# Optimization experiments

Measured on AMD Instinct MI355X. Metric: run time of the kernel, lower is better.

## Reference

```python
import jax, jax.numpy as jnp
import numpy as np

B, N, NC = 8, 25200, 80           # YOLOv5-640 / COCO raw output
CONF_THRES = 0.25                  # init conf_threshold
IOU_THRES = 0.45                   # init iou_threshold
PATCH_CONF = 0.001                 # hard-coded patch_conf in forward
GN = jnp.array([640.0, 640.0, 640.0, 640.0], dtype=jnp.float32)  # img_size[[1,0,1,0]]
MAX_WH = 4096.0                    # class offset for class-aware NMS
K_CLEAN = 512                      # fixed-size cap on NMS candidates (clean branch)
K_PATCH = 1024                     # fixed-size cap on NMS candidates (patch branch)
MAX_DET_CLEAN = 1000
MAX_DET_PATCH = 30000
NEG = jnp.float32(-1e30)


def _xywh2xyxy(x):
    xy, wh = x[..., :2], x[..., 2:4]
    return jnp.concatenate([xy - wh * 0.5, xy + wh * 0.5], axis=-1)


def _pairwise_iou(a, b):
    # a: [A,4] xyxy, b: [B,4] xyxy -> [A,B] jaccard overlap
    tl = jnp.maximum(a[:, None, :2], b[None, :, :2])
    br = jnp.minimum(a[:, None, 2:4], b[None, :, 2:4])
    wh = jnp.clip(br - tl, 0.0)
    inter = wh[..., 0] * wh[..., 1]
    area_a = (a[:, 2] - a[:, 0]) * (a[:, 3] - a[:, 1])
    area_b = (b[:, 2] - b[:, 0]) * (b[:, 3] - b[:, 1])
    union = area_a[:, None] + area_b[None, :] - inter
    union = jnp.where(union > 0, union, 1.0)  # guard degenerate boxes
    return inter / union


def _nms_single(pred, conf_thres, K, max_det):
    # pred: [N, 5+nc]. Fixed-size (padded/masked) greedy NMS, class-aware via MAX_WH offset.
    obj = pred[:, 4]
    cls_conf = pred[:, 5:] * obj[:, None]          # x[:,5:] *= x[:,4:5]
    conf = jnp.max(cls_conf, axis=-1)
    cls = jnp.argmax(cls_conf, axis=-1)
    box = _xywh2xyxy(pred[:, :4])
    valid = (obj > conf_thres) & (conf > conf_thres)
    scores = jnp.where(valid, conf, NEG)
    top_scores, idx = jax.lax.top_k(scores, K)     # sorted desc, like torchvision NMS ordering
    boxes = box[idx]
    cls_k = cls[idx]
    valid_k = top_scores > conf_thres
    boxes_off = boxes + cls_k.astype(boxes.dtype)[:, None] * MAX_WH
    iou = jax.lax.stop_gradient(_pairwise_iou(boxes_off, boxes_off))
    ar = jnp.arange(K)

    def step(keep, i):
        sup = keep[i] & (iou[i] > IOU_THRES) & (ar > i)
        return keep & (~sup), None

    keep, _ = jax.lax.scan(step, valid_k, jnp.arange(K))
    rank = jnp.cumsum(keep.astype(jnp.int32))
    keep = keep & (rank <= max_det)
    return boxes, cls_k, keep


def _image_loss(cb, cc, ck, pb, pc, pk):
    # per clean detection: max IoU over kept patch boxes of the same class (0 if none)
    iou = _pairwise_iou(cb / GN, pb / GN)          # [K_CLEAN, K_PATCH]
    mask = ck[:, None] & pk[None, :] & (cc[:, None] == pc[None, :])
    tm = jnp.max(jnp.where(mask, iou, 0.0), axis=1)
    s = jnp.sum(jnp.where(ck, tm, 0.0))
    n = jnp.sum(ck.astype(jnp.float32))
    return s, n


def _forward(output_clean, output_patch):
    cb, cc, ck = jax.vmap(lambda p: _nms_single(p, CONF_THRES, K_CLEAN, MAX_DET_CLEAN))(output_clean)
    pb, pc, pk = jax.vmap(lambda p: _nms_single(p, PATCH_CONF, K_PATCH, MAX_DET_PATCH))(output_patch)
    s, n = jax.vmap(_image_loss)(cb, cc, ck, pb, pc, pk)
    total, cnt = jnp.sum(s), jnp.sum(n)
    return jnp.where(cnt > 0, 1.0 - total / jnp.maximum(cnt, 1.0), jnp.float32(1.0))


def _make_pred(key):
    ka, kb, kc, kd = jax.random.split(key, 4)
    cxcy = jax.random.uniform(ka, (B, N, 2), jnp.float32, 20.0, 620.0)
    wh = jax.random.uniform(kb, (B, N, 2), jnp.float32, 2.0, 150.0)
    obj = jax.random.uniform(kc, (B, N, 1), jnp.float32)
    clsp = jax.random.uniform(kd, (B, N, NC), jnp.float32)
    return jnp.concatenate([cxcy, wh, obj, clsp], axis=-1)


def setup_inputs() -> dict:
    key = jax.random.key(0)
    k1, k2 = jax.random.split(key)
    return {"output_clean": _make_pred(k1), "output_patch": _make_pred(k2)}


def reference(output_clean, output_patch):
    return _forward(output_clean, output_patch)
```

## Files before the change

kernel.cpp:

```cpp
#include <hip/hip_runtime.h>


static constexpr int NB   = 8;
static constexpr int NA   = 25200;
static constexpr int NCLS = 80;
static constexpr int CH   = 85;
static constexpr int NT   = 16;
static constexpr int KMAX = 1024;
static constexpr int NBIN = 32768;
static constexpr int PSH  = 17;
static constexpr int CAP  = 2048;
static constexpr int CPAD = 32;
static constexpr int IOB  = 34;

static constexpr size_t OFF_KEYS = 0;
static constexpr size_t OFF_CLS  = OFF_KEYS + (size_t)NT * NA * 4;
static constexpr size_t OFF_BOX  = OFF_CLS  + (size_t)NT * NA * 4;
static constexpr size_t OFF_CLSK = OFF_BOX  + (size_t)NT * KMAX * 16;
static constexpr size_t OFF_VALK = OFF_CLSK + (size_t)NT * KMAX * 4;
static constexpr size_t OFF_KEEP = OFF_VALK + (size_t)NT * KMAX * 4;
static constexpr size_t OFF_SUP  = OFF_KEEP + (size_t)NT * 16 * 8;
static constexpr size_t OFF_DIAG = OFF_SUP  + (size_t)NT * KMAX * 16 * 8;
static constexpr size_t OFF_PART = OFF_DIAG + (size_t)NT * KMAX * 8;
static constexpr size_t OFF_CNT  = OFF_PART + 512;
static constexpr size_t OFF_THR  = OFF_CNT  + (size_t)NT * 2 * CPAD * 4;
static constexpr size_t OFF_CAND = OFF_THR  + 128;

__device__ __forceinline__ unsigned okey(float f) {
  unsigned u = __float_as_uint(f);
  return (u & 0x80000000u) ? ~u : (u | 0x80000000u);
}

__global__ __launch_bounds__(256) void k_score(const float* __restrict__ clean,
                                               const float* __restrict__ patch,
                                               unsigned* __restrict__ keys,
                                               int* __restrict__ clsArr) {
#pragma clang fp contract(off)
  const int t  = blockIdx.y;
  const int a0 = blockIdx.x * 64;
  const int nA = (NA - a0 < 64) ? (NA - a0) : 64;
  const float conf_th = (t < 8) ? 0.25f : 0.001f;
  const float* __restrict__ src = ((t < 8) ? clean : patch) + (size_t)(t & 7) * NA * CH;
  __shared__ float rows[64 * CH];
  const float4* g4 = (const float4*)(src + (size_t)a0 * CH);
  float4* s4 = (float4*)rows;
  const int n4 = (nA * CH) >> 2;
  for (int i = threadIdx.x; i < n4; i += 256) s4[i] = g4[i];
  __syncthreads();

  const int ar = threadIdx.x >> 2;
  const int q  = threadIdx.x & 3;
  if (ar < nA) {
    const float* r = rows + ar * CH;
    const float obj = r[4];
    const int c0 = q * 20;
    float best = r[5 + c0] * obj;
    int bc = c0;
    for (int c = c0 + 1; c < c0 + 20; ++c) {
      float v = r[5 + c] * obj;
      if (v > best) { best = v; bc = c; }
    }
    {
      float b2 = __shfl_down(best, 2); int c2 = __shfl_down(bc, 2);
      if (b2 > best || (b2 == best && c2 < bc)) { best = b2; bc = c2; }
      float b1 = __shfl_down(best, 1); int c1 = __shfl_down(bc, 1);
      if (b1 > best || (b1 == best && c1 < bc)) { best = b1; bc = c1; }
    }
    if (q == 0) {
      const bool valid = (obj > conf_th) && (best > conf_th);
      const float score = valid ? best : -1e30f;
      const int a = a0 + ar;
      keys[(size_t)t * NA + a]   = okey(score);
      clsArr[(size_t)t * NA + a] = bc;
    }
  }
}

__global__ __launch_bounds__(1024) void k_histsel(const unsigned* __restrict__ keys,
                                                  unsigned* __restrict__ thr,
                                                  unsigned* __restrict__ cnt) {
  const int t = blockIdx.x;
  const unsigned K = (t < 8) ? 512u : 1024u;
  __shared__ unsigned h32[NBIN / 2];
  __shared__ unsigned csum[1024];
  __shared__ int s_chunk;
  __shared__ unsigned s_acc;
  const int tid = threadIdx.x;
  for (int i = tid; i < NBIN / 2; i += 1024) h32[i] = 0u;
  if (tid < 2) cnt[(t * 2 + tid) * CPAD] = 0u;
  __syncthreads();
  const unsigned INVKEY = okey(-1e30f);
  const unsigned* kv = keys + (size_t)t * NA;
  const int lane = tid & 63;
  for (int i = tid; i < NA; i += 1024) {
    unsigned key = kv[i];
    bool inv = (key == INVKEY);
    unsigned long long mb = __ballot(inv);
    if (!inv) {
      unsigned b = key >> PSH;
      atomicAdd(&h32[b >> 1], 1u << ((b & 1) * 16));
    } else if (lane == (int)__ffsll(mb) - 1) {
      unsigned b = INVKEY >> PSH;
      atomicAdd(&h32[b >> 1], (unsigned)__popcll(mb) << ((b & 1) * 16));
    }
  }
  __syncthreads();
  {
    unsigned sum = 0;
    for (int i = 0; i < 16; ++i) {
      unsigned v = h32[tid * 16 + i];
      sum += (v & 0xFFFFu) + (v >> 16);
    }
    csum[tid] = sum;
  }
  __syncthreads();
  for (int off = 1; off < 1024; off <<= 1) {
    unsigned v = csum[tid];
    if (tid + off < 1024) v += csum[tid + off];
    __syncthreads();
    csum[tid] = v;
    __syncthreads();
  }
  {
    bool pred = csum[tid] >= K;
    bool next = (tid == 1023) ? false : (csum[tid + 1] >= K);
    if (pred && !next) {
      s_chunk = tid;
      s_acc = (tid == 1023) ? 0u : csum[tid + 1];
    }
  }
  __syncthreads();
  if (tid == 0) {
    unsigned acc = s_acc;
    unsigned res = (unsigned)(s_chunk * 32);
    for (int i = 31; i >= 0; --i) {
      int bb = s_chunk * 32 + i;
      unsigned v = h32[bb >> 1];
      unsigned c2 = (bb & 1) ? (v >> 16) : (v & 0xFFFFu);
      if (acc + c2 >= K) { res = (unsigned)bb; break; }
      acc += c2;
    }
    thr[t] = res;
  }
}

__global__ __launch_bounds__(256) void k_compact(const unsigned* __restrict__ keys,
                                                 const unsigned* __restrict__ thr,
                                                 unsigned* __restrict__ cnt,
                                                 unsigned long long* __restrict__ cand) {
  const int t = blockIdx.y;
  const int a = blockIdx.x * 256 + threadIdx.x;
  const unsigned B = thr[t];
  unsigned key = 0u, p = 0u;
  const bool inb = (a < NA);
  if (inb) { key = keys[(size_t)t * NA + a]; p = key >> PSH; }
  const bool hi = inb && (p > B);
  const bool eq = inb && (p == B);
  const unsigned long long item =
      ((unsigned long long)key << 32) | (unsigned)(~(unsigned)a);
  const int lane = threadIdx.x & 63;
  const unsigned long long lowmask =
      (lane == 0) ? 0ull : (0xFFFFFFFFFFFFFFFFull >> (64 - lane));
  unsigned long long mh = __ballot(hi);
  if (mh) {
    const int leader = (int)__ffsll(mh) - 1;
    unsigned base = 0;
    if (lane == leader) base = atomicAdd(&cnt[(t * 2 + 0) * CPAD], (unsigned)__popcll(mh));
    base = __shfl(base, leader);
    if (hi) {
      unsigned pos = base + (unsigned)__popcll(mh & lowmask);
      if (pos < 1024u) cand[(size_t)t * CAP + pos] = item;
    }
  }
  unsigned long long me = __ballot(eq);
  if (me) {
    const int leader = (int)__ffsll(me) - 1;
    unsigned base = 0;
    if (lane == leader) base = atomicAdd(&cnt[(t * 2 + 1) * CPAD], (unsigned)__popcll(me));
    base = __shfl(base, leader);
    if (eq) {
      unsigned pos = base + (unsigned)__popcll(me & lowmask);
      if (pos < 1024u) cand[(size_t)t * CAP + 1024 + pos] = item;
    }
  }
}

__global__ __launch_bounds__(1024) void k_sort(const float* __restrict__ clean,
                                               const float* __restrict__ patch,
                                               const unsigned* __restrict__ cnt,
                                               const unsigned long long* __restrict__ cand,
                                               const int* __restrict__ clsArr,
                                               float* __restrict__ boxesK,
                                               int* __restrict__ clsK,
                                               int* __restrict__ validK) {
#pragma clang fp contract(off)
  const int t = blockIdx.x;
  const int K = (t < 8) ? 512 : 1024;
  const float conf_th = (t < 8) ? 0.25f : 0.001f;
  __shared__ unsigned long long buf[CAP];
  const unsigned nHi = min(cnt[(t * 2 + 0) * CPAD], 1024u);
  const unsigned nEq = min(cnt[(t * 2 + 1) * CPAD], 1024u);
  const unsigned long long* cd = cand + (size_t)t * CAP;
  for (int i = threadIdx.x; i < CAP; i += 1024) {
    unsigned long long v = 0ull;
    if (i < 1024) { if ((unsigned)i < nHi) v = cd[i]; }
    else          { if ((unsigned)(i - 1024) < nEq) v = cd[i]; }
    buf[i] = v;
  }
  __syncthreads();
  for (int kk2 = 2; kk2 <= CAP; kk2 <<= 1) {
    for (int j = kk2 >> 1; j > 0; j >>= 1) {
      for (int i = threadIdx.x; i < CAP; i += 1024) {
        int ixj = i ^ j;
        if (ixj > i) {
          unsigned long long a = buf[i], b = buf[ixj];
          bool desc = ((i & kk2) == 0);
          if (desc ? (a < b) : (a > b)) { buf[i] = b; buf[ixj] = a; }
        }
      }
      __syncthreads();
    }
  }
  const float* __restrict__ src = ((t < 8) ? clean : patch) + (size_t)(t & 7) * NA * CH;
  const unsigned vkey = okey(conf_th);
  for (int k = threadIdx.x; k < K; k += 1024) {
    unsigned long long v = buf[k];
    unsigned key = (unsigned)(v >> 32);
    int idx = (int)(~(unsigned)(v & 0xFFFFFFFFull));
    if (idx < 0) idx = 0;
    const float* r = src + (size_t)idx * CH;
    float cx = r[0], cy = r[1], w = r[2], h = r[3];
    float hw = w * 0.5f, hh = h * 0.5f;
    float* bo = boxesK + ((size_t)t * KMAX + k) * 4;
    bo[0] = cx - hw; bo[1] = cy - hh; bo[2] = cx + hw; bo[3] = cy + hh;
    clsK[t * KMAX + k]   = clsArr[(size_t)t * NA + idx];
    validK[t * KMAX + k] = (key > vkey) ? 1 : 0;
  }
}

__global__ __launch_bounds__(256) void k_ioumat(const float* __restrict__ boxesK,
                                                const int* __restrict__ clsK,
                                                unsigned long long* __restrict__ sup,
                                                unsigned long long* __restrict__ diag) {
#pragma clang fp contract(off)
  const int t  = blockIdx.y;
  const int K  = (t < 8) ? 512 : 1024;
  const int lw = (t < 8) ? 3 : 4;
  const int nw = 1 << lw;
  const int npair = (nw * (nw + 1)) / 2;
  const int total = npair * 64;
  if (blockIdx.x * 256 >= total) return;
  __shared__ float X1[KMAX + 16], Y1[KMAX + 16], X2[KMAX + 16], Y2[KMAX + 16], AR[KMAX + 16];
  for (int i = threadIdx.x; i < K; i += 256) {
    const float* bo = boxesK + ((size_t)t * KMAX + i) * 4;
    float off = (float)clsK[t * KMAX + i] * 4096.0f;
    float x1 = bo[0] + off, y1 = bo[1] + off, x2 = bo[2] + off, y2 = bo[3] + off;
    const int ip = i + (i >> 6);
    X1[ip] = x1; Y1[ip] = y1; X2[ip] = x2; Y2[ip] = y2;
    AR[ip] = (x2 - x1) * (y2 - y1);
  }
  __syncthreads();
  unsigned long long* supt = sup + (size_t)t * (KMAX * 16);
  for (int widx = blockIdx.x * 256 + threadIdx.x; widx < total; widx += IOB * 256) {
    int p = widx >> 6;
    int row = widx & 63;
    int rb = 0, pr = p;
    while (pr >= nw - rb) { pr -= nw - rb; ++rb; }
    const int wc = rb + pr;
    const int i = rb * 64 + row;
    const int ipi = i + rb;
    const float x1i = X1[ipi], y1i = Y1[ipi], x2i = X2[ipi], y2i = Y2[ipi], ai = AR[ipi];
    unsigned long long m = 0ull;
    const int jb = (wc << 6) + wc;
    const bool offd = (wc > rb);
#pragma unroll 4
    for (int l = 0; l < 64; ++l) {
      const int jp = jb + l;
      float tlx = fmaxf(x1i, X1[jp]);
      float tly = fmaxf(y1i, Y1[jp]);
      float brx = fminf(x2i, X2[jp]);
      float bry = fminf(y2i, Y2[jp]);
      float w = fmaxf(brx - tlx, 0.0f);
      float h = fmaxf(bry - tly, 0.0f);
      float inter = w * h;
      float uni = (ai + AR[jp]) - inter;
      uni = (uni > 0.0f) ? uni : 1.0f;
      float iou = inter / uni;
      bool hit = (iou > 0.45f) && (offd || ((wc << 6) + l > i));
      m |= hit ? (1ull << l) : 0ull;
    }
    supt[(size_t)i * nw + wc] = m;
    if (wc == rb) diag[(size_t)t * KMAX + i] = m;
  }
}

__global__ __launch_bounds__(64) void k_greedy(const unsigned long long* __restrict__ sup,
                                               const unsigned long long* __restrict__ diag,
                                               const int* __restrict__ validK,
                                               unsigned long long* __restrict__ keepw) {
  const int t  = blockIdx.x;
  const int K  = (t < 8) ? 512 : 1024;
  const int lw = (t < 8) ? 3 : 4;
  const int nw = 1 << lw;
  const int lane = threadIdx.x;
  __shared__ unsigned long long sdiag[KMAX];
  const unsigned long long* dg = diag + (size_t)t * KMAX;
  for (int i = lane; i < K; i += 64) sdiag[i] = dg[i];
  int v16[16];
#pragma unroll
  for (int W = 0; W < 16; ++W)
    v16[W] = (W < nw) ? validK[t * KMAX + W * 64 + lane] : 0;
  unsigned long long vkeep = 0ull;
#pragma unroll
  for (int W = 0; W < 16; ++W)
    if (W < nw) {
      unsigned long long bl = __ballot(v16[W] != 0);
      if (lane == W) vkeep = bl;
    }
  __syncthreads();
  const int w = lane & (nw - 1);
  const int b = lane >> lw;
  const unsigned long long* base = sup + (size_t)t * (KMAX * 16);
  unsigned long long remv = 0ull;
  for (int W = 0; W < nw; ++W) {
    unsigned long long cur = __shfl(vkeep, W) & ~__shfl(remv, W);
    for (int rb = 0; rb < 64; rb += 16) {
      unsigned long long tm[16];
#pragma unroll
      for (int i2 = 0; i2 < 16; ++i2) tm[i2] = sdiag[W * 64 + rb + i2];
#pragma unroll
      for (int i2 = 0; i2 < 16; ++i2) {
        unsigned long long msk = 0ull - ((cur >> (rb + i2)) & 1ull);
        cur &= ~(tm[i2] & msk);
      }
    }
    if (lane == 0) keepw[t * 16 + W] = cur;
    if (W + 1 < nw) {
      const int r0 = b * nw;
      unsigned long long vv[16];
#pragma unroll
      for (int j = 0; j < 16; ++j) {
        bool take = (j < nw) && (w > W) && ((cur >> (r0 + j)) & 1ull);
        vv[j] = take ? base[(size_t)(W * 64 + r0 + j) * nw + w] : 0ull;
      }
      unsigned long long part = 0ull;
#pragma unroll
      for (int j = 0; j < 16; ++j) part |= vv[j];
      for (int s = nw; s < 64; s <<= 1) part |= __shfl_xor(part, s);
      remv |= part;
    }
  }
}

__global__ __launch_bounds__(1024) void k_loss(const float* __restrict__ boxesK,
                                               const int* __restrict__ clsK,
                                               const unsigned long long* __restrict__ keepw,
                                               float* __restrict__ part) {
#pragma clang fp contract(off)
  const int img = blockIdx.y;
  const int chunk = blockIdx.x;
  const int tp = 8 + img;
  __shared__ float px1[KMAX], py1[KMAX], px2[KMAX], py2[KMAX], pa[KMAX];
  __shared__ int pcls[KMAX];
  __shared__ float red[1024];
  for (int j = threadIdx.x; j < KMAX; j += 1024) {
    const float* bo = boxesK + ((size_t)tp * KMAX + j) * 4;
    float x1 = bo[0] / 640.0f, y1 = bo[1] / 640.0f;
    float x2 = bo[2] / 640.0f, y2 = bo[3] / 640.0f;
    px1[j] = x1; py1[j] = y1; px2[j] = x2; py2[j] = y2;
    pa[j] = (x2 - x1) * (y2 - y1);
    int kept = (int)((keepw[tp * 16 + (j >> 6)] >> (j & 63)) & 1ull);
    pcls[j] = kept ? clsK[tp * KMAX + j] : -1;
  }
  __syncthreads();
  const int row = chunk * 64 + (threadIdx.x & 63);
  const int stripe = threadIdx.x >> 6;
  const int ck = (int)((keepw[img * 16 + (row >> 6)] >> (row & 63)) & 1ull);
  const float* bo = boxesK + ((size_t)img * KMAX + row) * 4;
  float cx1 = bo[0] / 640.0f, cy1 = bo[1] / 640.0f;
  float cx2 = bo[2] / 640.0f, cy2 = bo[3] / 640.0f;
  float ca = (cx2 - cx1) * (cy2 - cy1);
  const int ccls = clsK[img * KMAX + row];
  float m = 0.0f;
  if (ck) {
    const int j0 = stripe * 64;
    for (int j = j0; j < j0 + 64; ++j) {
      if (pcls[j] == ccls) {
        float tlx = fmaxf(cx1, px1[j]);
        float tly = fmaxf(cy1, py1[j]);
        float brx = fminf(cx2, px2[j]);
        float bry = fminf(cy2, py2[j]);
        float w = fmaxf(brx - tlx, 0.0f);
        float h = fmaxf(bry - tly, 0.0f);
        float inter = w * h;
        float uni = (ca + pa[j]) - inter;
        uni = (uni > 0.0f) ? uni : 1.0f;
        m = fmaxf(m, inter / uni);
      }
    }
  }
  red[threadIdx.x] = m;
  __syncthreads();
  if (threadIdx.x < 64) {
    float mm = red[threadIdx.x];
#pragma unroll
    for (int s = 1; s < 16; ++s) mm = fmaxf(mm, red[threadIdx.x + 64 * s]);
    float sv = ck ? mm : 0.0f;
    float nv = ck ? 1.0f : 0.0f;
    for (int off = 32; off > 0; off >>= 1) {
      sv += __shfl_down(sv, off);
      nv += __shfl_down(nv, off);
    }
    if (threadIdx.x == 0) {
      int b = img * 8 + chunk;
      part[b * 2 + 0] = sv;
      part[b * 2 + 1] = nv;
    }
  }
}

__global__ __launch_bounds__(64) void k_final(const float* __restrict__ part,
                                              float* __restrict__ out) {
  int lane = threadIdx.x;
  float sv = part[lane * 2 + 0];
  float nv = part[lane * 2 + 1];
  for (int off = 32; off > 0; off >>= 1) {
    sv += __shfl_down(sv, off);
    nv += __shfl_down(nv, off);
  }
  if (lane == 0) out[0] = (nv > 0.0f) ? (1.0f - sv / fmaxf(nv, 1.0f)) : 1.0f;
}

extern "C" void kernel_launch(void* const* d_in, const int* in_sizes, int n_in,
                              void* d_out, int out_size, void* d_ws, size_t ws_size,
                              hipStream_t stream) {
  const float* clean = (const float*)d_in[0];
  const float* patch = (const float*)d_in[1];
  char* ws = (char*)d_ws;
  unsigned* keys            = (unsigned*)(ws + OFF_KEYS);
  int* clsArr               = (int*)(ws + OFF_CLS);
  float* boxesK             = (float*)(ws + OFF_BOX);
  int* clsK                 = (int*)(ws + OFF_CLSK);
  int* validK               = (int*)(ws + OFF_VALK);
  unsigned long long* keepw = (unsigned long long*)(ws + OFF_KEEP);
  unsigned long long* sup   = (unsigned long long*)(ws + OFF_SUP);
  unsigned long long* diag  = (unsigned long long*)(ws + OFF_DIAG);
  float* part               = (float*)(ws + OFF_PART);
  unsigned* cnt             = (unsigned*)(ws + OFF_CNT);
  unsigned* thr             = (unsigned*)(ws + OFF_THR);
  unsigned long long* cand  = (unsigned long long*)(ws + OFF_CAND);
  float* out                = (float*)d_out;

  k_score  <<<dim3((NA + 63) / 64, NT), 256, 0, stream>>>(clean, patch, keys, clsArr);
  k_histsel<<<NT, 1024, 0, stream>>>(keys, thr, cnt);
  k_compact<<<dim3((NA + 255) / 256, NT), 256, 0, stream>>>(keys, thr, cnt, cand);
  k_sort   <<<NT, 1024, 0, stream>>>(clean, patch, cnt, cand, clsArr, boxesK, clsK, validK);
  k_ioumat <<<dim3(IOB, NT), 256, 0, stream>>>(boxesK, clsK, sup, diag);
  k_greedy <<<NT, 64, 0, stream>>>(sup, diag, validK, keepw);
  k_loss   <<<dim3(8, NB), 1024, 0, stream>>>(boxesK, clsK, keepw, part);
  k_final  <<<1, 64, 0, stream>>>(part, out);
}
```

Before: 278.0 us.

## Fuse histogram select, compaction and sort into one top-k kernel; async LDS loads

Merges the histogram threshold kernel, the grid-wide compaction kernel and the bitonic sort kernel into a single per-task block. Candidates are compacted straight into shared memory with shared atomics, so the global candidate and counter buffers and two kernel launches go away. The prefix scan switches from a 1024-step shared-memory loop to a wave shuffle plus a 16-way suffix. The score kernel now uses global_load_lds to copy rows directly into LDS. The cost is that compaction now runs on only 16 blocks instead of a wide grid, so parallelism is lower there.

New measurement: 275.0 us. About the same (-1.1%).

```diff
diff --git a/kernel.cpp b/kernel.cpp
--- a/kernel.cpp
+++ b/kernel.cpp
@@ -10,7 +10,6 @@
 static constexpr int NBIN = 32768;
 static constexpr int PSH  = 17;
 static constexpr int CAP  = 2048;
-static constexpr int CPAD = 32;
 static constexpr int IOB  = 34;
 
 static constexpr size_t OFF_KEYS = 0;
@@ -22,9 +21,6 @@
 static constexpr size_t OFF_SUP  = OFF_KEEP + (size_t)NT * 16 * 8;
 static constexpr size_t OFF_DIAG = OFF_SUP  + (size_t)NT * KMAX * 16 * 8;
 static constexpr size_t OFF_PART = OFF_DIAG + (size_t)NT * KMAX * 8;
-static constexpr size_t OFF_CNT  = OFF_PART + 512;
-static constexpr size_t OFF_THR  = OFF_CNT  + (size_t)NT * 2 * CPAD * 4;
-static constexpr size_t OFF_CAND = OFF_THR  + 128;
 
 __device__ __forceinline__ unsigned okey(float f) {
   unsigned u = __float_as_uint(f);
@@ -43,9 +39,20 @@
   const float* __restrict__ src = ((t < 8) ? clean : patch) + (size_t)(t & 7) * NA * CH;
   __shared__ float rows[64 * CH];
   const float4* g4 = (const float4*)(src + (size_t)a0 * CH);
-  float4* s4 = (float4*)rows;
+  float4* rows4 = (float4*)rows;
   const int n4 = (nA * CH) >> 2;
-  for (int i = threadIdx.x; i < n4; i += 256) s4[i] = g4[i];
+  const int wave = threadIdx.x >> 6;
+  const int lane = threadIdx.x & 63;
+  const int nchunk = (n4 + 63) >> 6;
+  for (int c = wave; c < nchunk; c += 4) {
+    const int i = (c << 6) + lane;
+    if (i < n4) {
+      __builtin_amdgcn_global_load_lds(
+          (const __attribute__((address_space(1))) void*)(g4 + i),
+          (__attribute__((address_space(3))) void*)(rows4 + (c << 6)),
+          16, 0, 0);
+    }
+  }
   __syncthreads();
 
   const int ar = threadIdx.x >> 2;
@@ -76,59 +83,65 @@
   }
 }
 
-__global__ __launch_bounds__(1024) void k_histsel(const unsigned* __restrict__ keys,
-                                                  unsigned* __restrict__ thr,
-                                                  unsigned* __restrict__ cnt) {
+__global__ __launch_bounds__(1024) void k_topsel(const unsigned* __restrict__ keys,
+                                                 const int* __restrict__ clsArr,
+                                                 const float* __restrict__ clean,
+                                                 const float* __restrict__ patch,
+                                                 float* __restrict__ boxesK,
+                                                 int* __restrict__ clsK,
+                                                 int* __restrict__ validK) {
+#pragma clang fp contract(off)
   const int t = blockIdx.x;
   const unsigned K = (t < 8) ? 512u : 1024u;
+  const float conf_th = (t < 8) ? 0.25f : 0.001f;
   __shared__ unsigned h32[NBIN / 2];
-  __shared__ unsigned csum[1024];
+  __shared__ unsigned long long buf[CAP];
+  __shared__ unsigned scnt[2];
+  __shared__ unsigned wtot[16], wsuf[16];
   __shared__ int s_chunk;
-  __shared__ unsigned s_acc;
+  __shared__ unsigned s_acc, s_B;
   const int tid = threadIdx.x;
+  const int lane = tid & 63, wv = tid >> 6;
   for (int i = tid; i < NBIN / 2; i += 1024) h32[i] = 0u;
-  if (tid < 2) cnt[(t * 2 + tid) * CPAD] = 0u;
+  for (int i = tid; i < CAP; i += 1024) buf[i] = 0ull;
+  if (tid < 2) scnt[tid] = 0u;
   __syncthreads();
   const unsigned INVKEY = okey(-1e30f);
   const unsigned* kv = keys + (size_t)t * NA;
-  const int lane = tid & 63;
-  for (int i = tid; i < NA; i += 1024) {
-    unsigned key = kv[i];
-    bool inv = (key == INVKEY);
+  for (int i = tid; i < 25600; i += 1024) {
+    const bool inb = (i < NA);
+    unsigned key = inb ? kv[i] : 0u;
+    const bool inv = inb && (key == INVKEY);
     unsigned long long mb = __ballot(inv);
-    if (!inv) {
+    if (inb && !inv) {
       unsigned b = key >> PSH;
       atomicAdd(&h32[b >> 1], 1u << ((b & 1) * 16));
-    } else if (lane == (int)__ffsll(mb) - 1) {
+    } else if (inv && lane == (int)__ffsll(mb) - 1) {
       unsigned b = INVKEY >> PSH;
       atomicAdd(&h32[b >> 1], (unsigned)__popcll(mb) << ((b & 1) * 16));
     }
   }
   __syncthreads();
-  {
-    unsigned sum = 0;
-    for (int i = 0; i < 16; ++i) {
-      unsigned v = h32[tid * 16 + i];
-      sum += (v & 0xFFFFu) + (v >> 16);
-    }
-    csum[tid] = sum;
-  }
-  __syncthreads();
-  for (int off = 1; off < 1024; off <<= 1) {
-    unsigned v = csum[tid];
-    if (tid + off < 1024) v += csum[tid + off];
-    __syncthreads();
-    csum[tid] = v;
-    __syncthreads();
-  }
-  {
-    bool pred = csum[tid] >= K;
-    bool next = (tid == 1023) ? false : (csum[tid + 1] >= K);
-    if (pred && !next) {
-      s_chunk = tid;
-      s_acc = (tid == 1023) ? 0u : csum[tid + 1];
-    }
-  }
+  unsigned cnt_c = 0;
+  for (int i = 0; i < 16; ++i) {
+    unsigned v = h32[tid * 16 + i];
+    cnt_c += (v & 0xFFFFu) + (v >> 16);
+  }
+  unsigned s = cnt_c;
+  for (int off = 1; off < 64; off <<= 1) {
+    unsigned v = __shfl_down(s, off);
+    if (lane + off < 64) s += v;
+  }
+  if (lane == 0) wtot[wv] = s;
+  __syncthreads();
+  if (tid < 16) {
+    unsigned acc = 0;
+    for (int w2 = 15; w2 > tid; --w2) acc += wtot[w2];
+    wsuf[tid] = acc;
+  }
+  __syncthreads();
+  const unsigned suf = s + wsuf[wv];
+  if (suf >= K && suf - cnt_c < K) { s_chunk = tid; s_acc = suf - cnt_c; }
   __syncthreads();
   if (tid == 0) {
     unsigned acc = s_acc;
@@ -140,77 +153,47 @@
       if (acc + c2 >= K) { res = (unsigned)bb; break; }
       acc += c2;
     }
-    thr[t] = res;
-  }
-}
-
-__global__ __launch_bounds__(256) void k_compact(const unsigned* __restrict__ keys,
-                                                 const unsigned* __restrict__ thr,
-                                                 unsigned* __restrict__ cnt,
-                                                 unsigned long long* __restrict__ cand) {
-  const int t = blockIdx.y;
-  const int a = blockIdx.x * 256 + threadIdx.x;
-  const unsigned B = thr[t];
-  unsigned key = 0u, p = 0u;
-  const bool inb = (a < NA);
-  if (inb) { key = keys[(size_t)t * NA + a]; p = key >> PSH; }
-  const bool hi = inb && (p > B);
-  const bool eq = inb && (p == B);
-  const unsigned long long item =
-      ((unsigned long long)key << 32) | (unsigned)(~(unsigned)a);
-  const int lane = threadIdx.x & 63;
+    s_B = res;
+  }
+  __syncthreads();
+  const unsigned B = s_B;
   const unsigned long long lowmask =
       (lane == 0) ? 0ull : (0xFFFFFFFFFFFFFFFFull >> (64 - lane));
-  unsigned long long mh = __ballot(hi);
-  if (mh) {
-    const int leader = (int)__ffsll(mh) - 1;
-    unsigned base = 0;
-    if (lane == leader) base = atomicAdd(&cnt[(t * 2 + 0) * CPAD], (unsigned)__popcll(mh));
-    base = __shfl(base, leader);
-    if (hi) {
-      unsigned pos = base + (unsigned)__popcll(mh & lowmask);
-      if (pos < 1024u) cand[(size_t)t * CAP + pos] = item;
-    }
-  }
-  unsigned long long me = __ballot(eq);
-  if (me) {
-    const int leader = (int)__ffsll(me) - 1;
-    unsigned base = 0;
-    if (lane == leader) base = atomicAdd(&cnt[(t * 2 + 1) * CPAD], (unsigned)__popcll(me));
-    base = __shfl(base, leader);
-    if (eq) {
-      unsigned pos = base + (unsigned)__popcll(me & lowmask);
-      if (pos < 1024u) cand[(size_t)t * CAP + 1024 + pos] = item;
-    }
-  }
-}
-
-__global__ __launch_bounds__(1024) void k_sort(const float* __restrict__ clean,
-                                               const float* __restrict__ patch,
-                                               const unsigned* __restrict__ cnt,
-                                               const unsigned long long* __restrict__ cand,
-                                               const int* __restrict__ clsArr,
-                                               float* __restrict__ boxesK,
-                                               int* __restrict__ clsK,
-                                               int* __restrict__ validK) {
-#pragma clang fp contract(off)
-  const int t = blockIdx.x;
-  const int K = (t < 8) ? 512 : 1024;
-  const float conf_th = (t < 8) ? 0.25f : 0.001f;
-  __shared__ unsigned long long buf[CAP];
-  const unsigned nHi = min(cnt[(t * 2 + 0) * CPAD], 1024u);
-  const unsigned nEq = min(cnt[(t * 2 + 1) * CPAD], 1024u);
-  const unsigned long long* cd = cand + (size_t)t * CAP;
-  for (int i = threadIdx.x; i < CAP; i += 1024) {
-    unsigned long long v = 0ull;
-    if (i < 1024) { if ((unsigned)i < nHi) v = cd[i]; }
-    else          { if ((unsigned)(i - 1024) < nEq) v = cd[i]; }
-    buf[i] = v;
+  for (int i = tid; i < 25600; i += 1024) {
+    const bool inb = (i < NA);
+    unsigned key = inb ? kv[i] : 0u;
+    unsigned p = key >> PSH;
+    const bool hi = inb && (p > B);
+    const bool eq = inb && (p == B);
+    const unsigned long long item =
+        ((unsigned long long)key << 32) | (unsigned)(~(unsigned)i);
+    unsigned long long mh = __ballot(hi);
+    if (mh) {
+      int leader = (int)__ffsll(mh) - 1;
+      unsigned base2 = 0;
+      if (lane == leader) base2 = atomicAdd(&scnt[0], (unsigned)__popcll(mh));
+      base2 = __shfl(base2, leader);
+      if (hi) {
+        unsigned pos = base2 + (unsigned)__popcll(mh & lowmask);
+        if (pos < 1024u) buf[pos] = item;
+      }
+    }
+    unsigned long long me = __ballot(eq);
+    if (me) {
+      int leader = (int)__ffsll(me) - 1;
+      unsigned base2 = 0;
+      if (lane == leader) base2 = atomicAdd(&scnt[1], (unsigned)__popcll(me));
+      base2 = __shfl(base2, leader);
+      if (eq) {
+        unsigned pos = base2 + (unsigned)__popcll(me & lowmask);
+        if (pos < 1024u) buf[1024 + pos] = item;
+      }
+    }
   }
   __syncthreads();
   for (int kk2 = 2; kk2 <= CAP; kk2 <<= 1) {
     for (int j = kk2 >> 1; j > 0; j >>= 1) {
-      for (int i = threadIdx.x; i < CAP; i += 1024) {
+      for (int i = tid; i < CAP; i += 1024) {
         int ixj = i ^ j;
         if (ixj > i) {
           unsigned long long a = buf[i], b = buf[ixj];
@@ -223,11 +206,11 @@
   }
   const float* __restrict__ src = ((t < 8) ? clean : patch) + (size_t)(t & 7) * NA * CH;
   const unsigned vkey = okey(conf_th);
-  for (int k = threadIdx.x; k < K; k += 1024) {
+  for (int k = tid; k < (int)K; k += 1024) {
     unsigned long long v = buf[k];
     unsigned key = (unsigned)(v >> 32);
     int idx = (int)(~(unsigned)(v & 0xFFFFFFFFull));
-    if (idx < 0) idx = 0;
+    if (idx < 0 || idx >= NA) idx = 0;
     const float* r = src + (size_t)idx * CH;
     float cx = r[0], cy = r[1], w = r[2], h = r[3];
     float hw = w * 0.5f, hh = h * 0.5f;
@@ -446,15 +429,10 @@
   unsigned long long* sup   = (unsigned long long*)(ws + OFF_SUP);
   unsigned long long* diag  = (unsigned long long*)(ws + OFF_DIAG);
   float* part               = (float*)(ws + OFF_PART);
-  unsigned* cnt             = (unsigned*)(ws + OFF_CNT);
-  unsigned* thr             = (unsigned*)(ws + OFF_THR);
-  unsigned long long* cand  = (unsigned long long*)(ws + OFF_CAND);
   float* out                = (float*)d_out;
 
   k_score  <<<dim3((NA + 63) / 64, NT), 256, 0, stream>>>(clean, patch, keys, clsArr);
-  k_histsel<<<NT, 1024, 0, stream>>>(keys, thr, cnt);
-  k_compact<<<dim3((NA + 255) / 256, NT), 256, 0, stream>>>(keys, thr, cnt, cand);
-  k_sort   <<<NT, 1024, 0, stream>>>(clean, patch, cnt, cand, clsArr, boxesK, clsK, validK);
+  k_topsel <<<NT, 1024, 0, stream>>>(keys, clsArr, clean, patch, boxesK, clsK, validK);
   k_ioumat <<<dim3(IOB, NT), 256, 0, stream>>>(boxesK, clsK, sup, diag);
   k_greedy <<<NT, 64, 0, stream>>>(sup, diag, validK, keepw);
   k_loss   <<<dim3(8, NB), 1024, 0, stream>>>(boxesK, clsK, keepw, part);
```
